# Performance work log

Measured on AMD Instinct MI355X. Metric: run time of the kernel, lower is better.

The kernel has to match this reference:

```python
import jax, jax.numpy as jnp
import numpy as np

N_NODES = 100000
N_EDGES = 1600000
F_IN = 64
HID = 64
N_CLASSES = 45
N_GRAPHS = 256


def gcn_conv(x, src, dst, W, b, n):
    # GCNConv with added self-loops and symmetric normalization (PyG semantics)
    h = x @ W  # [N, H]
    deg = jax.ops.segment_sum(jnp.ones(src.shape[0], h.dtype), dst, num_segments=n) + 1.0
    dinv = jax.lax.rsqrt(deg)  # deg^{-1/2}, deg >= 1 due to self loops
    coef = dinv[src] * dinv[dst]  # [E]
    msg = h[src] * coef[:, None]  # gather + scale
    agg = jax.ops.segment_sum(msg, dst, num_segments=n)  # scatter-add to dst
    agg = agg + h * (dinv * dinv)[:, None]  # self-loop contribution
    return agg + b


def setup_inputs() -> dict:
    key = jax.random.key(0)
    ks = jax.random.split(key, 12)
    x = jax.random.normal(ks[0], (N_NODES, F_IN), dtype=jnp.float32)
    edge_index = jax.random.randint(ks[1], (2, N_EDGES), 0, N_NODES, dtype=jnp.int32)
    batch = jnp.sort(jax.random.randint(ks[2], (N_NODES,), 0, N_GRAPHS, dtype=jnp.int32))
    s1 = 1.0 / np.sqrt(F_IN)
    s2 = 1.0 / np.sqrt(HID)
    W1 = jax.random.uniform(ks[3], (F_IN, HID), jnp.float32, -s1, s1)
    b1 = jnp.zeros((HID,), jnp.float32)
    W2 = jax.random.uniform(ks[4], (HID, HID), jnp.float32, -s2, s2)
    b2 = jnp.zeros((HID,), jnp.float32)
    W3 = jax.random.uniform(ks[5], (HID, HID), jnp.float32, -s2, s2)
    b3 = jnp.zeros((HID,), jnp.float32)
    Wl = jax.random.uniform(ks[6], (HID, N_CLASSES), jnp.float32, -s2, s2)
    bl = jnp.zeros((N_CLASSES,), jnp.float32)
    return {"x": x, "edge_index": edge_index, "batch": batch,
            "W1": W1, "b1": b1, "W2": W2, "b2": b2, "W3": W3, "b3": b3,
            "Wl": Wl, "bl": bl}


def reference(x, edge_index, batch, W1, b1, W2, b2, W3, b3, Wl, bl):
    n = x.shape[0]
    src, dst = edge_index[0], edge_index[1]
    h = jax.nn.relu(gcn_conv(x, src, dst, W1, b1, n))
    h = jax.nn.relu(gcn_conv(h, src, dst, W2, b2, n))
    h = gcn_conv(h, src, dst, W3, b3, n)
    # global mean pool over graph segments
    sums = jax.ops.segment_sum(h, batch, num_segments=N_GRAPHS)  # [G, H]
    cnts = jax.ops.segment_sum(jnp.ones(n, h.dtype), batch, num_segments=N_GRAPHS)
    pooled = sums / jnp.maximum(cnts, 1.0)[:, None]
    # dropout is identity in eval mode
    return pooled @ Wl + bl  # [G, num_classes]
```

## Files before the change

### kernel.cpp

```cpp
#include <hip/hip_runtime.h>
#include <hip/hip_bf16.h>

#define N_NODES   100000
#define N_EDGES   1600000
#define F_IN      64
#define HID       64
#define N_CLASSES 45
#define N_GRAPHS  256
#define SB        196
#define NPB       512
#define CAP       9216
#define WPB       144
#define CHUNK     4096
#define NCHUNK    391
#define NZB       256
#define GEMM_GRID 3125
#define ZLEN4     3204096

__device__ __forceinline__ float rl_f(float v, int k) {
    return __uint_as_float(__builtin_amdgcn_readlane(__float_as_uint(v), k));
}
__device__ __forceinline__ int rl_i(int v, int k) {
    return __builtin_amdgcn_readlane(v, k);
}
__device__ __forceinline__ unsigned short f2bf(float x) {
    unsigned u = __float_as_uint(x);
    unsigned r = u + 0x7FFFu + ((u >> 16) & 1u);
    return (unsigned short)(r >> 16);
}
__device__ __forceinline__ float bf2f(unsigned short h) {
    return __uint_as_float(((unsigned)h) << 16);
}

__global__ __launch_bounds__(256) void k_front(const int* __restrict__ src, const int* __restrict__ dst,
                                               int* __restrict__ bcur, int* __restrict__ binned,
                                               const float* __restrict__ x, const float* __restrict__ W1,
                                               unsigned short* __restrict__ P, float* __restrict__ zbase) {
    int bid = blockIdx.x;
    int t   = threadIdx.x;
    if (bid < NCHUNK) {
        __shared__ int stg[CHUNK];
        __shared__ int dbuf[CHUNK];
        __shared__ int h[SB], lbase[SB], gbase[SB], cur[SB];
        __shared__ int ss[256];
        if (t < SB) h[t] = 0;
        __syncthreads();
        int base4 = bid * (CHUNK / 4);
        #pragma unroll
        for (int i = 0; i < CHUNK / 1024; i++) {
            int l4 = i * 256 + t;
            int e4 = base4 + l4;
            if (e4 < N_EDGES / 4) {
                int4 d = ((const int4*)dst)[e4];
                ((int4*)dbuf)[l4] = d;
                atomicAdd(&h[d.x >> 9], 1);
                atomicAdd(&h[d.y >> 9], 1);
                atomicAdd(&h[d.z >> 9], 1);
                atomicAdd(&h[d.w >> 9], 1);
            }
        }
        __syncthreads();
        ss[t] = (t < SB) ? h[t] : 0;
        __syncthreads();
        for (int o = 1; o < 256; o <<= 1) {
            int v = (t >= o) ? ss[t - o] : 0;
            __syncthreads();
            if (t >= o) ss[t] += v;
            __syncthreads();
        }
        if (t < SB) {
            int ex = ss[t] - h[t];
            lbase[t] = ex;
            cur[t]   = ex;
            gbase[t] = t * CAP + atomicAdd(&bcur[t], h[t]);
        }
        __syncthreads();
        #pragma unroll
        for (int i = 0; i < CHUNK / 1024; i++) {
            int l4 = i * 256 + t;
            int e4 = base4 + l4;
            if (e4 < N_EDGES / 4) {
                int4 s4 = ((const int4*)src)[e4];
                int4 d  = ((int4*)dbuf)[l4];
                int q;
                q = atomicAdd(&cur[d.x >> 9], 1); stg[q] = s4.x | ((d.x & 511) << 17);
                q = atomicAdd(&cur[d.y >> 9], 1); stg[q] = s4.y | ((d.y & 511) << 17);
                q = atomicAdd(&cur[d.z >> 9], 1); stg[q] = s4.z | ((d.z & 511) << 17);
                q = atomicAdd(&cur[d.w >> 9], 1); stg[q] = s4.w | ((d.w & 511) << 17);
            }
        }
        __syncthreads();
        int wv = t >> 6, lane = t & 63;
        for (int b = wv; b < SB; b += 4) {
            int n = h[b], lb = lbase[b], gb = gbase[b];
            for (int i = lane; i < n; i += 64)
                binned[gb + i] = stg[lb + i];
        }
    } else if (bid < NCHUNK + NZB) {
        float4 z = make_float4(0.f, 0.f, 0.f, 0.f);
        float4* zp = (float4*)zbase;
        int zb = bid - NCHUNK;
        for (long i = (long)zb * 256 + t; i < (long)ZLEN4; i += (long)NZB * 256)
            zp[i] = z;
    } else {
        int gbid = bid - NCHUNK - NZB;
        int lane = t & 63;
        int wv   = t >> 6;
        int base = gbid * 32 + wv * 8;
        float xr[8], acc[8];
        #pragma unroll
        for (int r = 0; r < 8; r++) {
            xr[r]  = x[(size_t)(base + r) * 64 + lane];
            acc[r] = 0.f;
        }
        for (int kb = 0; kb < 64; kb += 8) {
            float wb[8];
            #pragma unroll
            for (int j = 0; j < 8; j++) wb[j] = W1[(kb + j) * 64 + lane];
            #pragma unroll
            for (int j = 0; j < 8; j++) {
                #pragma unroll
                for (int r = 0; r < 8; r++)
                    acc[r] = fmaf(rl_f(xr[r], kb + j), wb[j], acc[r]);
            }
        }
        #pragma unroll
        for (int r = 0; r < 8; r++)
            P[(size_t)(base + r) * 64 + lane] = f2bf(acc[r]);
    }
}

__global__ __launch_bounds__(256) void k_bcsr(const int* __restrict__ binned, const int* __restrict__ bcur,
                                              float* __restrict__ dinv, float* __restrict__ dinv2,
                                              int* __restrict__ csr) {
    __shared__ int h[NPB];
    __shared__ int ts[256];
    int t = threadIdx.x;
    int b = blockIdx.x;
    int nb0  = b << 9;
    int ebeg = b * CAP;
    int ecnt = bcur[b]; if (ecnt > CAP) ecnt = CAP;
    h[t] = 0; h[t + 256] = 0;
    __syncthreads();
    for (int i = t; i < ecnt; i += 256)
        atomicAdd(&h[binned[ebeg + i] >> 17], 1);
    __syncthreads();
    int c0 = h[t * 2], c1 = h[t * 2 + 1];
    int tot = c0 + c1;
    ts[t] = tot;
    __syncthreads();
    for (int o = 1; o < 256; o <<= 1) {
        int v = (t >= o) ? ts[t - o] : 0;
        __syncthreads();
        if (t >= o) ts[t] += v;
        __syncthreads();
    }
    int ex = ts[t] - tot + ebeg;
    int n0 = nb0 + t * 2;
    int e0 = ex, e1 = ex + c0;
    if (n0 < N_NODES) {
        float i0 = 1.0f / (float)(c0 + 1);
        float i1 = 1.0f / (float)(c1 + 1);
        dinv2[n0]     = i0;  dinv2[n0 + 1] = i1;
        dinv[n0]      = sqrtf(i0);
        dinv[n0 + 1]  = sqrtf(i1);
    }
    __syncthreads();
    h[t * 2] = e0; h[t * 2 + 1] = e1;
    __syncthreads();
    for (int i = t; i < ecnt; i += 256) {
        int p = binned[ebeg + i];
        int q = atomicAdd(&h[p >> 17], 1);
        csr[q] = p;
    }
}

template<bool POOLI>
__global__ __launch_bounds__(256) void k_gemm(const float* __restrict__ E,
                                              unsigned short* P,
                                              const float* __restrict__ W,
                                              const float* __restrict__ bprev,
                                              const float* __restrict__ bcurr,
                                              const float* __restrict__ dinv2,
                                              const int* __restrict__ batch,
                                              float* __restrict__ pool) {
    int lane = threadIdx.x & 63;
    int wv   = threadIdx.x >> 6;
    int base = blockIdx.x * 32 + wv * 8;
    float bp = bprev[lane];
    float xr[8], acc[8];
    #pragma unroll
    for (int r = 0; r < 8; r++) {
        int n = base + r;
        float hp = bf2f(P[(size_t)n * 64 + lane]);
        float a  = E[(size_t)n * 64 + lane] + fmaf(hp, dinv2[n], bp);
        xr[r]  = fmaxf(a, 0.f);
        acc[r] = 0.f;
    }
    for (int kb = 0; kb < 64; kb += 8) {
        float wb[8];
        #pragma unroll
        for (int j = 0; j < 8; j++) wb[j] = W[(kb + j) * 64 + lane];
        #pragma unroll
        for (int j = 0; j < 8; j++) {
            #pragma unroll
            for (int r = 0; r < 8; r++)
                acc[r] = fmaf(rl_f(xr[r], kb + j), wb[j], acc[r]);
        }
    }
    #pragma unroll
    for (int r = 0; r < 8; r++)
        P[(size_t)(base + r) * 64 + lane] = f2bf(acc[r]);
    if (POOLI) {
        float bv = bcurr[lane];
        float d2[8];
        #pragma unroll
        for (int r = 0; r < 8; r++) d2[r] = dinv2[base + r];
        int g0 = batch[base], g7 = batch[base + 7];
        if (g0 == g7) {
            float s = 0.f;
            #pragma unroll
            for (int r = 0; r < 8; r++) s += fmaf(acc[r], d2[r], bv);
            atomicAdd(&pool[g0 * 64 + lane], s);
        } else {
            #pragma unroll
            for (int r = 0; r < 8; r++) {
                int g = batch[base + r];
                atomicAdd(&pool[g * 64 + lane], fmaf(acc[r], d2[r], bv));
            }
        }
    }
}

template<bool POOLEP>
__global__ __launch_bounds__(256, 8) void k_agge(const unsigned short* __restrict__ Hbuf,
                                                 const int* __restrict__ csr,
                                                 const int* __restrict__ bcur,
                                                 const float* __restrict__ dinv,
                                                 const int* __restrict__ batch,
                                                 float* __restrict__ Out) {
    int wv   = threadIdx.x >> 6;
    int lane = threadIdx.x & 63;
    int wid  = blockIdx.x * 4 + wv;
    int b    = wid / WPB;
    int lw   = wid - b * WPB;
    int used = bcur[b]; if (used > CAP) used = CAP;
    int e0   = lw * 64;
    int rem  = used - e0;
    if (rem <= 0) return;
    if (rem > 64) rem = 64;
    int base = b * CAP + e0;

    int p = 0;
    float cv = 0.f;
    if (lane < rem) {
        p  = csr[base + lane];
        cv = dinv[p & 0x1FFFF];
    }
    int sv = p & 0x1FFFF;
    int dv = p >> 17;
    if (rem < 64) {
        int dlast = rl_i(dv, rem - 1);
        if (lane >= rem) dv = dlast;
    }
    int dup = __shfl_up(dv, 1);
    unsigned long long bm = __ballot(lane > 0 && dv != dup);

    auto flush = [&](int dl, float a) {
        int dst = (b << 9) + dl;
        if (dst < N_NODES) {
            float val = dinv[dst] * a;
            if (POOLEP) {
                int g = batch[dst];
                atomicAdd(&Out[g * 64 + lane], val);
            } else {
                atomicAdd(&Out[(size_t)dst * 64 + lane], val);
            }
        }
    };

    int   curd = rl_i(dv, 0);
    float acc  = 0.f;
    unsigned short u[2][16];

    #pragma unroll
    for (int i = 0; i < 16; i++)
        u[0][i] = Hbuf[(size_t)rl_i(sv, i) * 64 + lane];
    #pragma unroll
    for (int blk = 0; blk < 4; blk++) {
        if (blk + 1 < 4) {
            #pragma unroll
            for (int i = 0; i < 16; i++)
                u[(blk + 1) & 1][i] = Hbuf[(size_t)rl_i(sv, (blk + 1) * 16 + i) * 64 + lane];
        }
        #pragma unroll
        for (int i = 0; i < 16; i++) {
            int e = blk * 16 + i;
            if ((bm >> e) & 1ull) {
                flush(curd, acc);
                acc  = 0.f;
                curd = rl_i(dv, e);
            }
            acc = fmaf(bf2f(u[blk & 1][i]), rl_f(cv, e), acc);
        }
    }
    flush(curd, acc);
}

__device__ __forceinline__ int lbound(const int* __restrict__ a, int n, int v) {
    int lo = 0, hi = n;
    while (lo < hi) { int m = (lo + hi) >> 1; if (a[m] < v) lo = m + 1; else hi = m; }
    return lo;
}

__global__ __launch_bounds__(64) void k_cls(const float* __restrict__ pool, const int* __restrict__ batch,
                                            const float* __restrict__ Wl, const float* __restrict__ bl,
                                            float* __restrict__ out) {
    __shared__ float pm[64];
    __shared__ int bounds[2];
    int g = blockIdx.x;
    int t = threadIdx.x;
    if (t < 2) bounds[t] = lbound(batch, N_NODES, g + t);
    __syncthreads();
    float cnt = (float)(bounds[1] - bounds[0]);
    pm[t] = pool[g * 64 + t] / fmaxf(cnt, 1.0f);
    __syncthreads();
    if (t < N_CLASSES) {
        float o = bl[t];
        #pragma unroll
        for (int k = 0; k < HID; k++) o = fmaf(pm[k], Wl[k * N_CLASSES + t], o);
        out[g * N_CLASSES + t] = o;
    }
}


extern "C" void kernel_launch(void* const* d_in, const int* in_sizes, int n_in,
                              void* d_out, int out_size, void* d_ws, size_t ws_size,
                              hipStream_t stream) {
    const float* x     = (const float*)d_in[0];
    const int*   eidx  = (const int*)  d_in[1];
    const int*   batch = (const int*)  d_in[2];
    const float* W1 = (const float*)d_in[3];
    const float* b1 = (const float*)d_in[4];
    const float* W2 = (const float*)d_in[5];
    const float* b2 = (const float*)d_in[6];
    const float* W3 = (const float*)d_in[7];
    const float* b3 = (const float*)d_in[8];
    const float* Wl = (const float*)d_in[9];
    const float* bl = (const float*)d_in[10];
    const int* src = eidx;
    const int* dst = eidx + N_EDGES;

    char* p = (char*)d_ws;
    auto alloc = [&](size_t bytes) -> void* {
        void* r = (void*)p;
        p += (bytes + 255) & ~(size_t)255;
        return r;
    };
    float* dinv  = (float*)alloc((size_t)N_NODES * 4);
    float* dinv2 = (float*)alloc((size_t)N_NODES * 4);
    int*   csr   = (int*)  alloc((size_t)SB * CAP * 4);
    unsigned short* P = (unsigned short*)alloc((size_t)N_NODES * 64 * 2);
    float* E1    = (float*)alloc((size_t)N_NODES * 64 * 4);
    float* pool  = (float*)alloc((size_t)N_GRAPHS * 64 * 4);
    float* E2    = (float*)alloc((size_t)N_NODES * 64 * 4);
    int*   bcur  = (int*)  alloc((size_t)SB * 4);
    int*   binned = (int*) alloc((size_t)SB * CAP * 4);

    const int agge_grid  = SB * WPB / 4;
    const int front_grid = NCHUNK + NZB + GEMM_GRID;

    hipMemsetAsync(bcur, 0, (size_t)SB * 4, stream);
    k_front<<<front_grid, 256, 0, stream>>>(src, dst, bcur, binned, x, W1, P, E1);
    k_bcsr <<<SB, 256, 0, stream>>>(binned, bcur, dinv, dinv2, csr);

    k_agge<false><<<agge_grid, 256, 0, stream>>>(P, csr, bcur, dinv, batch, E1);
    k_gemm<false><<<GEMM_GRID, 256, 0, stream>>>(E1, P, W2, b1, nullptr, dinv2, batch, nullptr);
    k_agge<false><<<agge_grid, 256, 0, stream>>>(P, csr, bcur, dinv, batch, E2);
    k_gemm<true ><<<GEMM_GRID, 256, 0, stream>>>(E2, P, W3, b2, b3, dinv2, batch, pool);
    k_agge<true ><<<agge_grid, 256, 0, stream>>>(P, csr, bcur, dinv, batch, pool);

    k_cls<<<N_GRAPHS, 64, 0, stream>>>(pool, batch, Wl, bl, (float*)d_out);
}
```

Measured before the change: 373.3 us.

## Halve destination bin size and restructure gather loop to process edges in groups of eight

Destination bins shrink from 512 to 256 nodes, which doubles the bin count and halves per-bin capacity. The front binning kernel, the CSR build and the aggregation indexing are all updated to match. The aggregation loop drops the ballot-based segment mask and its 64-edge double-buffered prefetch. It now reads eight edges at a time with early exit at the real edge count, comparing destinations with scalar readlane values. This trades the deeper prefetch pipeline for less wasted work on partial tiles and smaller bins, but the smaller capacity raises the risk of bin overflow.

```diff
diff --git a/kernel.cpp b/kernel.cpp
--- a/kernel.cpp
+++ b/kernel.cpp
@@ -7,10 +7,10 @@
 #define HID       64
 #define N_CLASSES 45
 #define N_GRAPHS  256
-#define SB        196
-#define NPB       512
-#define CAP       9216
-#define WPB       144
+#define SB        392
+#define NPB       256
+#define CAP       4608
+#define WPB       72
 #define CHUNK     4096
 #define NCHUNK    391
 #define NZB       256
@@ -41,9 +41,9 @@
     if (bid < NCHUNK) {
         __shared__ int stg[CHUNK];
         __shared__ int dbuf[CHUNK];
-        __shared__ int h[SB], lbase[SB], gbase[SB], cur[SB];
-        __shared__ int ss[256];
-        if (t < SB) h[t] = 0;
+        __shared__ int h[512], lb[512], gb[512], cur[512];
+        __shared__ int ps[256];
+        h[t] = 0; h[t + 256] = 0;
         __syncthreads();
         int base4 = bid * (CHUNK / 4);
         #pragma unroll
@@ -53,27 +53,28 @@
             if (e4 < N_EDGES / 4) {
                 int4 d = ((const int4*)dst)[e4];
                 ((int4*)dbuf)[l4] = d;
-                atomicAdd(&h[d.x >> 9], 1);
-                atomicAdd(&h[d.y >> 9], 1);
-                atomicAdd(&h[d.z >> 9], 1);
-                atomicAdd(&h[d.w >> 9], 1);
-            }
-        }
-        __syncthreads();
-        ss[t] = (t < SB) ? h[t] : 0;
+                atomicAdd(&h[d.x >> 8], 1);
+                atomicAdd(&h[d.y >> 8], 1);
+                atomicAdd(&h[d.z >> 8], 1);
+                atomicAdd(&h[d.w >> 8], 1);
+            }
+        }
+        __syncthreads();
+        int a0 = h[2 * t], a1 = h[2 * t + 1];
+        ps[t] = a0 + a1;
         __syncthreads();
         for (int o = 1; o < 256; o <<= 1) {
-            int v = (t >= o) ? ss[t - o] : 0;
+            int v = (t >= o) ? ps[t - o] : 0;
             __syncthreads();
-            if (t >= o) ss[t] += v;
+            if (t >= o) ps[t] += v;
             __syncthreads();
         }
-        if (t < SB) {
-            int ex = ss[t] - h[t];
-            lbase[t] = ex;
-            cur[t]   = ex;
-            gbase[t] = t * CAP + atomicAdd(&bcur[t], h[t]);
-        }
+        int pex = ps[t] - (a0 + a1);
+        int e0 = pex, e1 = pex + a0;
+        lb[2 * t] = e0;  lb[2 * t + 1] = e1;
+        cur[2 * t] = e0; cur[2 * t + 1] = e1;
+        if (2 * t < SB)     gb[2 * t]     = (2 * t) * CAP     + atomicAdd(&bcur[2 * t], a0);
+        if (2 * t + 1 < SB) gb[2 * t + 1] = (2 * t + 1) * CAP + atomicAdd(&bcur[2 * t + 1], a1);
         __syncthreads();
         #pragma unroll
         for (int i = 0; i < CHUNK / 1024; i++) {
@@ -83,18 +84,18 @@
                 int4 s4 = ((const int4*)src)[e4];
                 int4 d  = ((int4*)dbuf)[l4];
                 int q;
-                q = atomicAdd(&cur[d.x >> 9], 1); stg[q] = s4.x | ((d.x & 511) << 17);
-                q = atomicAdd(&cur[d.y >> 9], 1); stg[q] = s4.y | ((d.y & 511) << 17);
-                q = atomicAdd(&cur[d.z >> 9], 1); stg[q] = s4.z | ((d.z & 511) << 17);
-                q = atomicAdd(&cur[d.w >> 9], 1); stg[q] = s4.w | ((d.w & 511) << 17);
+                q = atomicAdd(&cur[d.x >> 8], 1); stg[q] = s4.x | ((d.x & 255) << 17);
+                q = atomicAdd(&cur[d.y >> 8], 1); stg[q] = s4.y | ((d.y & 255) << 17);
+                q = atomicAdd(&cur[d.z >> 8], 1); stg[q] = s4.z | ((d.z & 255) << 17);
+                q = atomicAdd(&cur[d.w >> 8], 1); stg[q] = s4.w | ((d.w & 255) << 17);
             }
         }
         __syncthreads();
         int wv = t >> 6, lane = t & 63;
         for (int b = wv; b < SB; b += 4) {
-            int n = h[b], lb = lbase[b], gb = gbase[b];
+            int n = h[b], l0 = lb[b], g0 = gb[b];
             for (int i = lane; i < n; i += 64)
-                binned[gb + i] = stg[lb + i];
+                binned[g0 + i] = stg[l0 + i];
         }
     } else if (bid < NCHUNK + NZB) {
         float4 z = make_float4(0.f, 0.f, 0.f, 0.f);
@@ -134,20 +135,19 @@
                                               float* __restrict__ dinv, float* __restrict__ dinv2,
                                               int* __restrict__ csr) {
     __shared__ int h[NPB];
-    __shared__ int ts[256];
+    __shared__ int ts[NPB];
     int t = threadIdx.x;
     int b = blockIdx.x;
-    int nb0  = b << 9;
+    int nb0  = b << 8;
     int ebeg = b * CAP;
     int ecnt = bcur[b]; if (ecnt > CAP) ecnt = CAP;
-    h[t] = 0; h[t + 256] = 0;
+    h[t] = 0;
     __syncthreads();
     for (int i = t; i < ecnt; i += 256)
         atomicAdd(&h[binned[ebeg + i] >> 17], 1);
     __syncthreads();
-    int c0 = h[t * 2], c1 = h[t * 2 + 1];
-    int tot = c0 + c1;
-    ts[t] = tot;
+    int c = h[t];
+    ts[t] = c;
     __syncthreads();
     for (int o = 1; o < 256; o <<= 1) {
         int v = (t >= o) ? ts[t - o] : 0;
@@ -155,18 +155,15 @@
         if (t >= o) ts[t] += v;
         __syncthreads();
     }
-    int ex = ts[t] - tot + ebeg;
-    int n0 = nb0 + t * 2;
-    int e0 = ex, e1 = ex + c0;
-    if (n0 < N_NODES) {
-        float i0 = 1.0f / (float)(c0 + 1);
-        float i1 = 1.0f / (float)(c1 + 1);
-        dinv2[n0]     = i0;  dinv2[n0 + 1] = i1;
-        dinv[n0]      = sqrtf(i0);
-        dinv[n0 + 1]  = sqrtf(i1);
-    }
-    __syncthreads();
-    h[t * 2] = e0; h[t * 2 + 1] = e1;
+    int excl = ts[t] - c + ebeg;
+    int n = nb0 + t;
+    if (n < N_NODES) {
+        float inv = 1.0f / (float)(c + 1);
+        dinv2[n] = inv;
+        dinv[n]  = sqrtf(inv);
+    }
+    __syncthreads();
+    h[t] = excl;
     __syncthreads();
     for (int i = t; i < ecnt; i += 256) {
         int p = binned[ebeg + i];
@@ -259,15 +256,9 @@
     }
     int sv = p & 0x1FFFF;
     int dv = p >> 17;
-    if (rem < 64) {
-        int dlast = rl_i(dv, rem - 1);
-        if (lane >= rem) dv = dlast;
-    }
-    int dup = __shfl_up(dv, 1);
-    unsigned long long bm = __ballot(lane > 0 && dv != dup);
 
     auto flush = [&](int dl, float a) {
-        int dst = (b << 9) + dl;
+        int dst = (b << 8) + dl;
         if (dst < N_NODES) {
             float val = dinv[dst] * a;
             if (POOLEP) {
@@ -279,32 +270,56 @@
         }
     };
 
-    int   curd = rl_i(dv, 0);
-    float acc  = 0.f;
-    unsigned short u[2][16];
-
-    #pragma unroll
-    for (int i = 0; i < 16; i++)
-        u[0][i] = Hbuf[(size_t)rl_i(sv, i) * 64 + lane];
-    #pragma unroll
-    for (int blk = 0; blk < 4; blk++) {
-        if (blk + 1 < 4) {
-            #pragma unroll
-            for (int i = 0; i < 16; i++)
-                u[(blk + 1) & 1][i] = Hbuf[(size_t)rl_i(sv, (blk + 1) * 16 + i) * 64 + lane];
-        }
-        #pragma unroll
-        for (int i = 0; i < 16; i++) {
-            int e = blk * 16 + i;
-            if ((bm >> e) & 1ull) {
-                flush(curd, acc);
-                acc  = 0.f;
-                curd = rl_i(dv, e);
-            }
-            acc = fmaf(bf2f(u[blk & 1][i]), rl_f(cv, e), acc);
-        }
-    }
-    flush(curd, acc);
+    int dprev = rl_i(dv, 0);
+    float acc = 0.f;
+    int j = 0;
+    for (; j + 8 <= rem; j += 8) {
+        int   s0 = rl_i(sv, j),     s1 = rl_i(sv, j + 1);
+        int   s2 = rl_i(sv, j + 2), s3 = rl_i(sv, j + 3);
+        int   s4 = rl_i(sv, j + 4), s5 = rl_i(sv, j + 5);
+        int   s6 = rl_i(sv, j + 6), s7 = rl_i(sv, j + 7);
+        float c0 = rl_f(cv, j),     c1 = rl_f(cv, j + 1);
+        float c2 = rl_f(cv, j + 2), c3 = rl_f(cv, j + 3);
+        float c4 = rl_f(cv, j + 4), c5 = rl_f(cv, j + 5);
+        float c6 = rl_f(cv, j + 6), c7 = rl_f(cv, j + 7);
+        int   d0 = rl_i(dv, j),     d1 = rl_i(dv, j + 1);
+        int   d2 = rl_i(dv, j + 2), d3 = rl_i(dv, j + 3);
+        int   d4 = rl_i(dv, j + 4), d5 = rl_i(dv, j + 5);
+        int   d6 = rl_i(dv, j + 6), d7 = rl_i(dv, j + 7);
+        unsigned short u0 = Hbuf[(size_t)s0 * 64 + lane];
+        unsigned short u1 = Hbuf[(size_t)s1 * 64 + lane];
+        unsigned short u2 = Hbuf[(size_t)s2 * 64 + lane];
+        unsigned short u3 = Hbuf[(size_t)s3 * 64 + lane];
+        unsigned short u4 = Hbuf[(size_t)s4 * 64 + lane];
+        unsigned short u5 = Hbuf[(size_t)s5 * 64 + lane];
+        unsigned short u6 = Hbuf[(size_t)s6 * 64 + lane];
+        unsigned short u7 = Hbuf[(size_t)s7 * 64 + lane];
+        if (d0 != dprev) { flush(dprev, acc); acc = 0.f; dprev = d0; }
+        acc = fmaf(bf2f(u0), c0, acc);
+        if (d1 != dprev) { flush(dprev, acc); acc = 0.f; dprev = d1; }
+        acc = fmaf(bf2f(u1), c1, acc);
+        if (d2 != dprev) { flush(dprev, acc); acc = 0.f; dprev = d2; }
+        acc = fmaf(bf2f(u2), c2, acc);
+        if (d3 != dprev) { flush(dprev, acc); acc = 0.f; dprev = d3; }
+        acc = fmaf(bf2f(u3), c3, acc);
+        if (d4 != dprev) { flush(dprev, acc); acc = 0.f; dprev = d4; }
+        acc = fmaf(bf2f(u4), c4, acc);
+        if (d5 != dprev) { flush(dprev, acc); acc = 0.f; dprev = d5; }
+        acc = fmaf(bf2f(u5), c5, acc);
+        if (d6 != dprev) { flush(dprev, acc); acc = 0.f; dprev = d6; }
+        acc = fmaf(bf2f(u6), c6, acc);
+        if (d7 != dprev) { flush(dprev, acc); acc = 0.f; dprev = d7; }
+        acc = fmaf(bf2f(u7), c7, acc);
+    }
+    for (; j < rem; j++) {
+        int   s0 = rl_i(sv, j);
+        float c0 = rl_f(cv, j);
+        int   d0 = rl_i(dv, j);
+        unsigned short u0 = Hbuf[(size_t)s0 * 64 + lane];
+        if (d0 != dprev) { flush(dprev, acc); acc = 0.f; dprev = d0; }
+        acc = fmaf(bf2f(u0), c0, acc);
+    }
+    flush(dprev, acc);
 }
 
 __device__ __forceinline__ int lbound(const int* __restrict__ a, int n, int v) {
```

Result: slower. 388.2 us (+4.0%).
